# Performance work log

Hardware: AMD Instinct MI355X
Metric: run time of the kernel (lower is better)

The kernel has to match this reference:

```python
import jax, jax.numpy as jnp
import numpy as np

WS = 7          # window_size
N = WS * WS     # 49 tokens per window
DIM = 384
H = 12
HD = DIM // H   # 32
NW = 64         # windows per image (mask leading dim)


def _rel_pos_index():
    coords = np.stack(np.meshgrid(np.arange(WS), np.arange(WS), indexing='ij'))  # (2, WS, WS)
    cf = coords.reshape(2, -1)                      # (2, N)
    rel = cf[:, :, None] - cf[:, None, :]           # (2, N, N)
    rel = rel.transpose(1, 2, 0)                    # (N, N, 2)
    idx = (rel[..., 0] + WS - 1) * (2 * WS - 1) + (rel[..., 1] + WS - 1)
    return jnp.asarray(idx, dtype=jnp.int32)        # (N, N)

REL_IDX = _rel_pos_index()


def setup_inputs() -> dict:
    key = jax.random.key(0)
    ks = jax.random.split(key, 10)
    B_ = 2048
    x = jax.random.normal(ks[0], (B_, N, DIM), dtype=jnp.float32)
    mask = jnp.zeros((NW, N, N), dtype=jnp.float32)
    s = 0.02
    Wq = jax.random.normal(ks[1], (DIM, DIM), jnp.float32) * s
    Wk = jax.random.normal(ks[2], (DIM, DIM), jnp.float32) * s
    Wv = jax.random.normal(ks[3], (DIM, DIM), jnp.float32) * s
    Wp = jax.random.normal(ks[4], (DIM, DIM), jnp.float32) * s
    bq = jnp.zeros((DIM,), jnp.float32)
    bk = jnp.zeros((DIM,), jnp.float32)
    bv = jnp.zeros((DIM,), jnp.float32)
    bp = jnp.zeros((DIM,), jnp.float32)
    table = jax.random.normal(ks[5], ((2 * WS - 1) ** 2, H), jnp.float32) * s
    return {"x": x, "mask": mask, "Wq": Wq, "bq": bq, "Wk": Wk, "bk": bk,
            "Wv": Wv, "bv": bv, "Wp": Wp, "bp": bp, "table": table}


def reference(x, mask, Wq, bq, Wk, bk, Wv, bv, Wp, bp, table):
    b_, n, c = x.shape
    scale = HD ** (-0.5)
    # projections: PyTorch Linear is x @ W.T + b
    q = (x @ Wq.T + bq).reshape(b_, n, H, HD).transpose(0, 2, 1, 3)  # (B, H, N, D)
    k = (x @ Wk.T + bk).reshape(b_, n, H, HD).transpose(0, 2, 1, 3)
    v = (x @ Wv.T + bv).reshape(b_, n, H, HD).transpose(0, 2, 1, 3)
    attn = jnp.einsum('bhnd,bhmd->bhnm', q * scale, k)               # (B, H, N, N)
    rel_bias = table[REL_IDX]                                        # (N, N, H)
    attn = attn + rel_bias.transpose(2, 0, 1)[None]                  # broadcast over B
    # mask add: (B//nW, nW, H, N, N) + mask[None, :, None]
    nw = mask.shape[0]
    attn = attn.reshape(b_ // nw, nw, H, n, n) + mask[None, :, None]
    attn = attn.reshape(b_, H, n, n)
    attn = jax.nn.softmax(attn, axis=-1)
    out = jnp.einsum('bhnm,bhmd->bhnd', attn, v)                     # (B, H, N, D)
    out = out.transpose(0, 2, 1, 3).reshape(b_, n, c)
    return out @ Wp.T + bp
```

## Files before the change

### kernel.cpp

```cpp
#include <hip/hip_runtime.h>
#include <stdint.h>

using bf16x8 = __attribute__((ext_vector_type(8))) short;
using f32x4  = __attribute__((ext_vector_type(4))) float;

__device__ __forceinline__ short f2bf(float f) {
  uint32_t u = __float_as_uint(f);
  u += 0x7fff + ((u >> 16) & 1u);
  return (short)(u >> 16);
}

#define MFMA16(a, b, c) __builtin_amdgcn_mfma_f32_16x16x32_bf16((a), (b), (c), 0, 0, 0)

__device__ __forceinline__ void gl_lds16(const short* g, short* l) {
  __builtin_amdgcn_global_load_lds(
      (const __attribute__((address_space(1))) void*)g,
      (__attribute__((address_space(3))) void*)l, 16, 0, 0);
}

__global__ void prep_w(const float* __restrict__ Wq, const float* __restrict__ bq,
                       const float* __restrict__ Wk, const float* __restrict__ bk,
                       const float* __restrict__ Wv, const float* __restrict__ bv,
                       const float* __restrict__ Wp, const float* __restrict__ bp,
                       short* __restrict__ Wqkv, short* __restrict__ Wpb,
                       float* __restrict__ bqkv, float* __restrict__ bpb) {
  int i = blockIdx.x * 256 + threadIdx.x;
  const float scale = 0.17677669529663687f;
  if (i < 1152 * 384) {
    int r = i / 384, k = i - r * 384;
    float v;
    if (r < 384)      v = Wq[r * 384 + k] * scale;
    else if (r < 768) v = Wk[(r - 384) * 384 + k];
    else              v = Wv[(r - 768) * 384 + k];
    Wqkv[i] = f2bf(v);
  }
  if (i < 384 * 384) Wpb[i] = f2bf(Wp[i]);
  if (i < 1152) bqkv[i] = (i < 384) ? bq[i] * scale : ((i < 768) ? bk[i - 384] : bv[i - 768]);
  if (i < 384) bpb[i] = bp[i];
}

__global__ void prep_bm(const float* __restrict__ table, const float* __restrict__ mask,
                        float* __restrict__ bmT, int nwmask) {
  int wm = blockIdx.x / 12, h = blockIdx.x - wm * 12;
  const float* mrow = mask + (size_t)wm * 2401;
  float* dst = bmT + (size_t)blockIdx.x * 4096;
  for (int e = threadIdx.x; e < 4096; e += 256) {
    int mn = e >> 8, cf = (e >> 4) & 15, if_ = e & 15;
    int row = (mn >> 2) * 16 + cf;
    int col = (mn & 3) * 16 + if_;
    float v = -3.0e38f;
    if (row < 49 && col < 49) {
      int id = row / 7, ir = row - id * 7;
      int jd = col / 7, jr = col - jd * 7;
      int idx = (id - jd + 6) * 13 + (ir - jr + 6);
      v = table[idx * 12 + h] + mrow[row * 49 + col];
    }
    dst[e] = v;
  }
}

__global__ __launch_bounds__(256) void qkv_gemm(
    const float* __restrict__ xf, const short* __restrict__ Wqkv,
    const float* __restrict__ bqkv,
    short* __restrict__ qws, short* __restrict__ kws, short* __restrict__ vws,
    int ntok) {
  __shared__ __align__(16) short smem[2 * 320 * 64];
  const int tid = threadIdx.x;
  const int lane = tid & 63, wv = tid >> 6;
  const int c = lane & 15, g = lane >> 4;

  const int mt = gridDim.y;
  int id = blockIdx.y * 6 + blockIdx.x;
  int mt8 = mt & ~7;
  int xq, yq;
  if (id < 6 * mt8) {
    int q = id / 48, r = id - q * 48;
    yq = q * 8 + (r & 7);
    xq = r >> 3;
  } else {
    int rem = id - 6 * mt8;
    xq = rem % 6;
    yq = mt8 + rem / 6;
  }
  const int n0 = xq * 192;
  const int row0 = yq * 128;

  f32x4 acc[8][3];
  const f32x4 zero = {0.f, 0.f, 0.f, 0.f};
#pragma unroll
  for (int m = 0; m < 8; m++)
#pragma unroll
    for (int nn = 0; nn < 3; nn++) acc[m][nn] = zero;

  const int rsub = lane >> 3;
  const int tchk = lane & 7;
  const int chnkB = ((lane & 7) ^ rsub) * 8;

  const float* aF[4];
  int aoff[4];
#pragma unroll
  for (int i = 0; i < 4; i++) {
    int r = (wv * 4 + i) * 8 + rsub;
    int grow = row0 + r;
    if (grow >= ntok) grow = ntok - 1;
    aF[i] = xf + (size_t)grow * 384 + tchk * 8;
    aoff[i] = r * 64 + ((tchk ^ rsub) * 8);
  }
  const short* bS[6];
#pragma unroll
  for (int j = 0; j < 6; j++) {
    int r = (wv * 6 + j) * 8 + rsub;
    bS[j] = Wqkv + (size_t)(n0 + r) * 384 + chnkB;
  }

  float4 a0[4], a1[4];
  auto loadA = [&](int ks) {
#pragma unroll
    for (int i = 0; i < 4; i++) {
      a0[i] = *(const float4*)(aF[i] + ks * 64);
      a1[i] = *(const float4*)(aF[i] + ks * 64 + 4);
    }
  };
  auto writeA = [&](int buf) {
    short* Asl = smem + buf * (320 * 64);
#pragma unroll
    for (int i = 0; i < 4; i++) {
      bf16x8 cv;
      cv[0] = f2bf(a0[i].x); cv[1] = f2bf(a0[i].y);
      cv[2] = f2bf(a0[i].z); cv[3] = f2bf(a0[i].w);
      cv[4] = f2bf(a1[i].x); cv[5] = f2bf(a1[i].y);
      cv[6] = f2bf(a1[i].z); cv[7] = f2bf(a1[i].w);
      *(bf16x8*)&Asl[aoff[i]] = cv;
    }
  };
  auto stageB = [&](int buf, int ks) {
    short* Bsl = smem + buf * (320 * 64) + 128 * 64;
#pragma unroll
    for (int j = 0; j < 6; j++)
      gl_lds16(bS[j] + ks * 64, Bsl + (wv * 6 + j) * 512);
  };

  loadA(0);
  stageB(0, 0);
  writeA(0);
  __syncthreads();
#pragma unroll
  for (int ks = 0; ks < 6; ks++) {
    const int cur = ks & 1;
    if (ks < 5) {
      loadA(ks + 1);
      stageB(cur ^ 1, ks + 1);
    }
    const short* Asl = smem + cur * (320 * 64);
    const short* Bsl = Asl + 128 * 64;
#pragma unroll
    for (int kk = 0; kk < 2; kk++) {
      bf16x8 af[8];
#pragma unroll
      for (int m = 0; m < 8; m++) {
        int row = m * 16 + c;
        af[m] = *(const bf16x8*)&Asl[row * 64 + (((kk * 4 + g) ^ (row & 7)) * 8)];
      }
#pragma unroll
      for (int nn = 0; nn < 3; nn++) {
        int row = wv * 48 + nn * 16 + c;
        bf16x8 bfr = *(const bf16x8*)&Bsl[row * 64 + (((kk * 4 + g) ^ (row & 7)) * 8)];
#pragma unroll
        for (int m = 0; m < 8; m++) acc[m][nn] = MFMA16(af[m], bfr, acc[m][nn]);
      }
    }
    if (ks < 5) writeA(cur ^ 1);
    __syncthreads();
  }

  const int s = n0 / 384;
  short* base = (s == 0) ? qws : ((s == 1) ? kws : vws);
  const int hbase = (n0 - s * 384) >> 5;
#pragma unroll
  for (int half = 0; half < 2; half++) {
    __syncthreads();
#pragma unroll
    for (int nn = 0; nn < 3; nn++) {
      int colRel = wv * 48 + nn * 16 + c;
      float bias = bqkv[n0 + colRel];
#pragma unroll
      for (int mm = 0; mm < 4; mm++) {
        int m = half * 4 + mm;
#pragma unroll
        for (int r = 0; r < 4; r++)
          smem[(mm * 16 + g * 4 + r) * 200 + colRel] = f2bf(acc[m][nn][r] + bias);
      }
    }
    __syncthreads();
    for (int u = tid; u < 384; u += 256) {
      int row = u & 63, j = u >> 6;
      int tr = row0 + half * 64 + row;
      if (tr < ntok) {
        int bw = tr / 49;
        int n = tr - bw * 49;
        short* dst = base + ((size_t)(bw * 12 + hbase + j) * 49 + n) * 32;
        const uint4* src = (const uint4*)&smem[row * 200 + j * 32];
        uint4* d4 = (uint4*)dst;
        d4[0] = src[0]; d4[1] = src[1]; d4[2] = src[2]; d4[3] = src[3];
      }
    }
  }
}

__global__ __launch_bounds__(256) void attn_kernel(
    const short* __restrict__ qws, const short* __restrict__ kws,
    const short* __restrict__ vws, short* __restrict__ ows,
    const float* __restrict__ bm, int b0, int nwmask) {
  __shared__ short Pall[4 * 64 * 72];
  const int tid = threadIdx.x;
  const int lane = tid & 63, wvi = tid >> 6;
  const int c = lane & 15, g = lane >> 4;
  const int task = blockIdx.x * 4 + wvi;
  const int b = task / 12, h = task - b * 12;
  const int wm = (b0 + b) % nwmask;
  const short* qb = qws + (size_t)(b * 12 + h) * 1568;
  const short* kb = kws + (size_t)(b * 12 + h) * 1568;
  const short* vb = vws + (size_t)(b * 12 + h) * 1568;

  bf16x8 qf[4], kf[4];
#pragma unroll
  for (int m = 0; m < 4; m++) { int i = m * 16 + c; if (i > 48) i = 48; qf[m] = *(const bf16x8*)(qb + i * 32 + g * 8); }
#pragma unroll
  for (int n = 0; n < 4; n++) { int j = n * 16 + c; if (j > 48) j = 48; kf[n] = *(const bf16x8*)(kb + j * 32 + g * 8); }

  bf16x8 vfr[2][2];
#pragma unroll
  for (int kk = 0; kk < 2; kk++)
#pragma unroll
    for (int dt = 0; dt < 2; dt++) {
      bf16x8 vf;
#pragma unroll
      for (int rr = 0; rr < 8; rr++) {
        int j = kk * 32 + g * 8 + rr; if (j > 48) j = 48;
        vf[rr] = vb[j * 32 + dt * 16 + c];
      }
      vfr[kk][dt] = vf;
    }

  const f32x4 zero = {0.f, 0.f, 0.f, 0.f};
  f32x4 S[4][4];
  __builtin_amdgcn_s_setprio(1);
#pragma unroll
  for (int m = 0; m < 4; m++)
#pragma unroll
    for (int n = 0; n < 4; n++) S[m][n] = MFMA16(kf[n], qf[m], zero);
  __builtin_amdgcn_s_setprio(0);

  const float* bmh = bm + (size_t)(wm * 12 + h) * 4096;
#pragma unroll
  for (int m = 0; m < 4; m++)
#pragma unroll
    for (int n = 0; n < 4; n++) {
      f32x4 b4 = *(const f32x4*)(bmh + ((m * 4 + n) * 16 + c) * 16 + g * 4);
      S[m][n][0] += b4[0]; S[m][n][1] += b4[1];
      S[m][n][2] += b4[2]; S[m][n][3] += b4[3];
    }

  short* P = Pall + wvi * 4608;
#pragma unroll
  for (int m = 0; m < 4; m++) {
    float mx = fmaxf(
        fmaxf(fmaxf(fmaxf(S[m][0][0], S[m][0][1]), fmaxf(S[m][0][2], S[m][0][3])),
              fmaxf(fmaxf(S[m][1][0], S[m][1][1]), fmaxf(S[m][1][2], S[m][1][3]))),
        fmaxf(fmaxf(fmaxf(S[m][2][0], S[m][2][1]), fmaxf(S[m][2][2], S[m][2][3])),
              fmaxf(fmaxf(S[m][3][0], S[m][3][1]), fmaxf(S[m][3][2], S[m][3][3]))));
    mx = fmaxf(mx, __shfl_xor(mx, 16));
    mx = fmaxf(mx, __shfl_xor(mx, 32));
    float e[4][4];
    float sm = 0.f;
#pragma unroll
    for (int n = 0; n < 4; n++)
#pragma unroll
      for (int r = 0; r < 4; r++) { e[n][r] = __expf(S[m][n][r] - mx); sm += e[n][r]; }
    sm += __shfl_xor(sm, 16);
    sm += __shfl_xor(sm, 32);
    float rv = 1.0f / sm;
#pragma unroll
    for (int n = 0; n < 4; n++) {
      uint32_t w0 = (uint32_t)(uint16_t)f2bf(e[n][0] * rv) |
                    ((uint32_t)(uint16_t)f2bf(e[n][1] * rv) << 16);
      uint32_t w1 = (uint32_t)(uint16_t)f2bf(e[n][2] * rv) |
                    ((uint32_t)(uint16_t)f2bf(e[n][3] * rv) << 16);
      uint2 w; w.x = w0; w.y = w1;
      *(uint2*)&P[(m * 16 + c) * 72 + n * 16 + g * 4] = w;
    }
  }

  f32x4 O[4][2];
#pragma unroll
  for (int m = 0; m < 4; m++) { O[m][0] = zero; O[m][1] = zero; }
#pragma unroll
  for (int kk = 0; kk < 2; kk++) {
    bf16x8 pf[4];
#pragma unroll
    for (int m = 0; m < 4; m++) pf[m] = *(const bf16x8*)&P[(m * 16 + c) * 72 + kk * 32 + g * 8];
    __builtin_amdgcn_s_setprio(1);
#pragma unroll
    for (int dt = 0; dt < 2; dt++)
#pragma unroll
      for (int m = 0; m < 4; m++) O[m][dt] = MFMA16(pf[m], vfr[kk][dt], O[m][dt]);
    __builtin_amdgcn_s_setprio(0);
  }
#pragma unroll
  for (int m = 0; m < 4; m++)
#pragma unroll
    for (int r = 0; r < 4; r++) {
      int i = m * 16 + g * 4 + r;
      if (i < 49) {
        size_t o = ((size_t)b * 49 + i) * 384 + h * 32;
        ows[o + c]      = f2bf(O[m][0][r]);
        ows[o + 16 + c] = f2bf(O[m][1][r]);
      }
    }
}

__global__ __launch_bounds__(256) void proj_gemm(
    const short* __restrict__ ows, const short* __restrict__ Wpb,
    const float* __restrict__ bpb, float* __restrict__ out,
    long tok0, int ntok) {
  __shared__ __align__(16) short smem[2 * 320 * 64];
  const int tid = threadIdx.x;
  const int lane = tid & 63, wv = tid >> 6;
  const int c = lane & 15, g = lane >> 4;

  const int mt = gridDim.y;
  int id = blockIdx.y * 2 + blockIdx.x;
  int mt8 = mt & ~7;
  int xq, yq;
  if (id < 2 * mt8) {
    int q = id / 16, r = id - q * 16;
    yq = q * 8 + (r & 7);
    xq = r >> 3;
  } else {
    int rem = id - 2 * mt8;
    xq = rem % 2;
    yq = mt8 + rem / 2;
  }
  const int n0 = xq * 192;
  const int row0 = yq * 128;

  f32x4 acc[8][3];
  const f32x4 zero = {0.f, 0.f, 0.f, 0.f};
#pragma unroll
  for (int m = 0; m < 8; m++)
#pragma unroll
    for (int nn = 0; nn < 3; nn++) acc[m][nn] = zero;

  const int rsub = lane >> 3;
  const int chnk = ((lane & 7) ^ rsub) * 8;
  const short* aS[4];
  const short* bS[6];
#pragma unroll
  for (int i = 0; i < 4; i++) {
    int r = (wv * 4 + i) * 8 + rsub;
    int grow = row0 + r;
    if (grow >= ntok) grow = ntok - 1;
    aS[i] = ows + (size_t)grow * 384 + chnk;
  }
#pragma unroll
  for (int j = 0; j < 6; j++) {
    int r = (wv * 6 + j) * 8 + rsub;
    bS[j] = Wpb + (size_t)(n0 + r) * 384 + chnk;
  }

  auto stage = [&](int buf, int ks) {
    short* Asl = smem + buf * (320 * 64);
    short* Bsl = Asl + 128 * 64;
#pragma unroll
    for (int i = 0; i < 4; i++)
      gl_lds16(aS[i] + ks * 64, Asl + (wv * 4 + i) * 512);
#pragma unroll
    for (int j = 0; j < 6; j++)
      gl_lds16(bS[j] + ks * 64, Bsl + (wv * 6 + j) * 512);
  };

  stage(0, 0);
  asm volatile("s_waitcnt vmcnt(0)" ::: "memory");
  __builtin_amdgcn_s_barrier();
#pragma unroll
  for (int ks = 0; ks < 6; ks++) {
    const int cur = ks & 1;
    if (ks < 5) {
      stage(cur ^ 1, ks + 1);
      asm volatile("s_waitcnt vmcnt(10)" ::: "memory");
    } else {
      asm volatile("s_waitcnt vmcnt(0)" ::: "memory");
    }
    __builtin_amdgcn_sched_barrier(0);
    __builtin_amdgcn_s_barrier();
    const short* Asl = smem + cur * (320 * 64);
    const short* Bsl = Asl + 128 * 64;
#pragma unroll
    for (int kk = 0; kk < 2; kk++) {
      bf16x8 af[8];
#pragma unroll
      for (int m = 0; m < 8; m++) {
        int row = m * 16 + c;
        af[m] = *(const bf16x8*)&Asl[row * 64 + (((kk * 4 + g) ^ (row & 7)) * 8)];
      }
#pragma unroll
      for (int nn = 0; nn < 3; nn++) {
        int row = wv * 48 + nn * 16 + c;
        bf16x8 bfr = *(const bf16x8*)&Bsl[row * 64 + (((kk * 4 + g) ^ (row & 7)) * 8)];
#pragma unroll
        for (int m = 0; m < 8; m++) acc[m][nn] = MFMA16(af[m], bfr, acc[m][nn]);
      }
    }
    __builtin_amdgcn_sched_barrier(0);
    __builtin_amdgcn_s_barrier();
  }

  float* fs = (float*)smem;
#pragma unroll
  for (int half = 0; half < 2; half++) {
    __syncthreads();
#pragma unroll
    for (int nn = 0; nn < 3; nn++) {
      int colRel = wv * 48 + nn * 16 + c;
      float bias = bpb[n0 + colRel];
#pragma unroll
      for (int mm = 0; mm < 4; mm++) {
        int m = half * 4 + mm;
#pragma unroll
        for (int r = 0; r < 4; r++)
          fs[(mm * 16 + g * 4 + r) * 196 + colRel] = acc[m][nn][r] + bias;
      }
    }
    __syncthreads();
#pragma unroll
    for (int t = 0; t < 12; t++) {
      int v = tid + t * 256;
      int row = v / 48, c4 = v - row * 48;
      int tr = row0 + half * 64 + row;
      if (tr < ntok)
        *(float4*)&out[(size_t)(tok0 + tr) * 384 + n0 + c4 * 4] =
            *(const float4*)&fs[row * 196 + c4 * 4];
    }
  }
}

extern "C" void kernel_launch(void* const* d_in, const int* in_sizes, int n_in,
                              void* d_out, int out_size, void* d_ws, size_t ws_size,
                              hipStream_t stream) {
  const float* x    = (const float*)d_in[0];
  const float* mask = (const float*)d_in[1];
  const float* Wq = (const float*)d_in[2];
  const float* bq = (const float*)d_in[3];
  const float* Wk = (const float*)d_in[4];
  const float* bk = (const float*)d_in[5];
  const float* Wv = (const float*)d_in[6];
  const float* bv = (const float*)d_in[7];
  const float* Wp = (const float*)d_in[8];
  const float* bp = (const float*)d_in[9];
  const float* table = (const float*)d_in[10];
  float* out = (float*)d_out;

  const int Btot = in_sizes[0] / (49 * 384);
  const int NWm  = in_sizes[1] / (49 * 49);

  char* ws = (char*)d_ws;
  short* Wqkv = (short*)ws;
  short* Wpb  = Wqkv + 1152 * 384;
  float* bqkv = (float*)(Wpb + 384 * 384);
  float* bpb  = bqkv + 1152;
  float* bmp  = bpb + 384;
  size_t fixedB = (size_t)(1152 * 384 + 384 * 384) * 2 + (1152 + 384) * 4
                + (size_t)NWm * 12 * 4096 * 4;
  char* dyn = ws + ((fixedB + 255) & ~(size_t)255);
  size_t used = (size_t)(dyn - ws);
  size_t avail = (ws_size > used + 4096) ? (ws_size - used - 4096) : 0;
  const size_t perw = (size_t)4 * 18816 * 2;
  long nwc = (long)(avail / perw);
  if (nwc > Btot) nwc = Btot;
  if (nwc >= 64) nwc &= ~63L;
  if (nwc < 1) nwc = 1;
  short* qws = (short*)dyn;
  short* kws = qws + (size_t)nwc * 18816;
  short* vws = kws + (size_t)nwc * 18816;
  short* ows = vws + (size_t)nwc * 18816;

  prep_w<<<dim3(1728), dim3(256), 0, stream>>>(Wq, bq, Wk, bk, Wv, bv, Wp, bp,
                                               Wqkv, Wpb, bqkv, bpb);
  prep_bm<<<dim3(NWm * 12), dim3(256), 0, stream>>>(table, mask, bmp, NWm);

  for (long b0 = 0; b0 < Btot; b0 += nwc) {
    int nw = (int)((Btot - b0 < nwc) ? (Btot - b0) : nwc);
    int ntok = nw * 49;
    long tok0 = b0 * 49;
    int mt = (ntok + 127) / 128;
    qkv_gemm<<<dim3(6, mt), dim3(256), 0, stream>>>(x + tok0 * 384, Wqkv, bqkv,
                                                    qws, kws, vws, ntok);
    attn_kernel<<<dim3(3 * nw), dim3(256), 0, stream>>>(qws, kws, vws, ows, bmp,
                                                        (int)b0, NWm);
    proj_gemm<<<dim3(2, mt), dim3(256), 0, stream>>>(ows, Wpb, bpb, out, tok0, ntok);
  }
}
```

Before: 570.5 us.

## Pre-convert x to bf16 and stage A tiles via direct global-to-LDS loads

Adds a separate prep_x kernel that converts the fp32 activations to bf16 in a workspace buffer. The QKV GEMM then stages both A and B tiles with global_load_lds, using explicit vmcnt waits and raw barriers in place of the register load, convert and LDS write path. The aim is to drop per-tile conversion work and register staging from the GEMM's inner loop and overlap loads better. The cost is an extra full read and write of x through HBM, plus a larger workspace per window that can shrink the chunk size.

```diff
diff --git a/kernel.cpp b/kernel.cpp
--- a/kernel.cpp
+++ b/kernel.cpp
@@ -59,8 +59,21 @@
   }
 }
 
+__global__ void prep_x(const float* __restrict__ x, short* __restrict__ xb, int n8) {
+  int u = blockIdx.x * 256 + threadIdx.x;
+  if (u < n8) {
+    int e = u * 8;
+    float4 f0 = *(const float4*)(x + e);
+    float4 f1 = *(const float4*)(x + e + 4);
+    bf16x8 cv;
+    cv[0] = f2bf(f0.x); cv[1] = f2bf(f0.y); cv[2] = f2bf(f0.z); cv[3] = f2bf(f0.w);
+    cv[4] = f2bf(f1.x); cv[5] = f2bf(f1.y); cv[6] = f2bf(f1.z); cv[7] = f2bf(f1.w);
+    *(bf16x8*)(xb + e) = cv;
+  }
+}
+
 __global__ __launch_bounds__(256) void qkv_gemm(
-    const float* __restrict__ xf, const short* __restrict__ Wqkv,
+    const short* __restrict__ xb, const short* __restrict__ Wqkv,
     const float* __restrict__ bqkv,
     short* __restrict__ qws, short* __restrict__ kws, short* __restrict__ vws,
     int ntok) {
@@ -93,64 +106,47 @@
     for (int nn = 0; nn < 3; nn++) acc[m][nn] = zero;
 
   const int rsub = lane >> 3;
-  const int tchk = lane & 7;
-  const int chnkB = ((lane & 7) ^ rsub) * 8;
-
-  const float* aF[4];
-  int aoff[4];
+  const int chnk = ((lane & 7) ^ rsub) * 8;
+  const short* aS[4];
+  const short* bS[6];
 #pragma unroll
   for (int i = 0; i < 4; i++) {
     int r = (wv * 4 + i) * 8 + rsub;
     int grow = row0 + r;
     if (grow >= ntok) grow = ntok - 1;
-    aF[i] = xf + (size_t)grow * 384 + tchk * 8;
-    aoff[i] = r * 64 + ((tchk ^ rsub) * 8);
-  }
-  const short* bS[6];
+    aS[i] = xb + (size_t)grow * 384 + chnk;
+  }
 #pragma unroll
   for (int j = 0; j < 6; j++) {
     int r = (wv * 6 + j) * 8 + rsub;
-    bS[j] = Wqkv + (size_t)(n0 + r) * 384 + chnkB;
-  }
-
-  float4 a0[4], a1[4];
-  auto loadA = [&](int ks) {
-#pragma unroll
-    for (int i = 0; i < 4; i++) {
-      a0[i] = *(const float4*)(aF[i] + ks * 64);
-      a1[i] = *(const float4*)(aF[i] + ks * 64 + 4);
-    }
-  };
-  auto writeA = [&](int buf) {
+    bS[j] = Wqkv + (size_t)(n0 + r) * 384 + chnk;
+  }
+
+  auto stage = [&](int buf, int ks) {
     short* Asl = smem + buf * (320 * 64);
-#pragma unroll
-    for (int i = 0; i < 4; i++) {
-      bf16x8 cv;
-      cv[0] = f2bf(a0[i].x); cv[1] = f2bf(a0[i].y);
-      cv[2] = f2bf(a0[i].z); cv[3] = f2bf(a0[i].w);
-      cv[4] = f2bf(a1[i].x); cv[5] = f2bf(a1[i].y);
-      cv[6] = f2bf(a1[i].z); cv[7] = f2bf(a1[i].w);
-      *(bf16x8*)&Asl[aoff[i]] = cv;
-    }
-  };
-  auto stageB = [&](int buf, int ks) {
-    short* Bsl = smem + buf * (320 * 64) + 128 * 64;
+    short* Bsl = Asl + 128 * 64;
+#pragma unroll
+    for (int i = 0; i < 4; i++)
+      gl_lds16(aS[i] + ks * 64, Asl + (wv * 4 + i) * 512);
 #pragma unroll
     for (int j = 0; j < 6; j++)
       gl_lds16(bS[j] + ks * 64, Bsl + (wv * 6 + j) * 512);
   };
 
-  loadA(0);
-  stageB(0, 0);
-  writeA(0);
-  __syncthreads();
+  stage(0, 0);
+  asm volatile("s_waitcnt vmcnt(0)" ::: "memory");
+  __builtin_amdgcn_s_barrier();
 #pragma unroll
   for (int ks = 0; ks < 6; ks++) {
     const int cur = ks & 1;
     if (ks < 5) {
-      loadA(ks + 1);
-      stageB(cur ^ 1, ks + 1);
-    }
+      stage(cur ^ 1, ks + 1);
+      asm volatile("s_waitcnt vmcnt(10)" ::: "memory");
+    } else {
+      asm volatile("s_waitcnt vmcnt(0)" ::: "memory");
+    }
+    __builtin_amdgcn_sched_barrier(0);
+    __builtin_amdgcn_s_barrier();
     const short* Asl = smem + cur * (320 * 64);
     const short* Bsl = Asl + 128 * 64;
 #pragma unroll
@@ -169,8 +165,8 @@
         for (int m = 0; m < 8; m++) acc[m][nn] = MFMA16(af[m], bfr, acc[m][nn]);
       }
     }
-    if (ks < 5) writeA(cur ^ 1);
-    __syncthreads();
+    __builtin_amdgcn_sched_barrier(0);
+    __builtin_amdgcn_s_barrier();
   }
 
   const int s = n0 / 384;
@@ -474,12 +470,13 @@
   char* dyn = ws + ((fixedB + 255) & ~(size_t)255);
   size_t used = (size_t)(dyn - ws);
   size_t avail = (ws_size > used + 4096) ? (ws_size - used - 4096) : 0;
-  const size_t perw = (size_t)4 * 18816 * 2;
+  const size_t perw = (size_t)5 * 18816 * 2;
   long nwc = (long)(avail / perw);
   if (nwc > Btot) nwc = Btot;
   if (nwc >= 64) nwc &= ~63L;
   if (nwc < 1) nwc = 1;
-  short* qws = (short*)dyn;
+  short* xbw = (short*)dyn;
+  short* qws = xbw + (size_t)nwc * 18816;
   short* kws = qws + (size_t)nwc * 18816;
   short* vws = kws + (size_t)nwc * 18816;
   short* ows = vws + (size_t)nwc * 18816;
@@ -492,9 +489,10 @@
     int nw = (int)((Btot - b0 < nwc) ? (Btot - b0) : nwc);
     int ntok = nw * 49;
     long tok0 = b0 * 49;
+    int n8 = ntok * 48;
+    prep_x<<<dim3((n8 + 255) / 256), dim3(256), 0, stream>>>(x + tok0 * 384, xbw, n8);
     int mt = (ntok + 127) / 128;
-    qkv_gemm<<<dim3(6, mt), dim3(256), 0, stream>>>(x + tok0 * 384, Wqkv, bqkv,
-                                                    qws, kws, vws, ntok);
+    qkv_gemm<<<dim3(6, mt), dim3(256), 0, stream>>>(xbw, Wqkv, bqkv, qws, kws, vws, ntok);
     attn_kernel<<<dim3(3 * nw), dim3(256), 0, stream>>>(qws, kws, vws, ows, bmp,
                                                         (int)b0, NWm);
     proj_gemm<<<dim3(2, mt), dim3(256), 0, stream>>>(ows, Wpb, bpb, out, tok0, ntok);
```

Measured after the change: 543.8 us. -4.7%, faster.
